# Kernel optimization log

Hardware: AMD Instinct MI355X
Metric: run time of the kernel (lower is better)

Reference implementation:

```python
import jax, jax.numpy as jnp
import numpy as np

EMBEDDING_DIM = 64
NUM_EMBEDDINGS = 512
COMMITMENT_COST = 0.25


def setup_inputs() -> dict:
    key = jax.random.key(0)
    k_x, k_w = jax.random.split(key)
    x = jax.random.normal(k_x, (32, 64, 64, EMBEDDING_DIM), dtype=jnp.float32)
    # he_normal initializer: stddev = sqrt(2 / fan_in), fan_in = embedding_dim
    emb_w = jax.random.normal(k_w, (NUM_EMBEDDINGS, EMBEDDING_DIM), dtype=jnp.float32) * jnp.sqrt(2.0 / EMBEDDING_DIM)
    return {"x": x, "emb_w": emb_w}


def reference(x, emb_w):
    D = emb_w.shape[1]
    K = emb_w.shape[0]
    flat = x.reshape(-1, D)  # [N, D]
    distances = (
        jnp.sum(flat * flat, axis=1, keepdims=True)
        - 2.0 * (flat @ emb_w.T)
        + jnp.sum(emb_w * emb_w, axis=1)[None, :]
    )
    # original: argmax(-distances) == argmin(distances)
    encoding_indices = jnp.argmin(distances, axis=1)  # [N]
    encodings = jax.nn.one_hot(encoding_indices, K, dtype=x.dtype)  # [N, K]
    quantized = emb_w[encoding_indices].reshape(x.shape)  # [B, H, W, D]

    sg = jax.lax.stop_gradient
    inp_latent_loss = jnp.mean((sg(quantized) - x) ** 2)
    emb_latent_loss = jnp.mean((quantized - sg(x)) ** 2)
    loss = emb_latent_loss + COMMITMENT_COST * inp_latent_loss

    # straight-through estimator
    quantized_st = x + sg(quantized - x)

    avg_probs = jnp.mean(encodings, axis=0)  # [K]
    perplexity = jnp.exp(-jnp.sum(avg_probs * jnp.log(avg_probs + 1e-10)))
    return (loss, quantized_st, perplexity, encodings)
```

## Files before the change

### kernel.cpp

```cpp
#include <hip/hip_runtime.h>
#include <math.h>

#define NVEC 131072
#define DIM 64
#define KCB 512
#define FLT_BIG 3.402823466e38f

typedef __attribute__((ext_vector_type(8))) short bf16x8;
typedef __attribute__((ext_vector_type(4))) float f32x4;
typedef __attribute__((ext_vector_type(2))) float f32x2;


__device__ inline unsigned int bf16_rne(float f) {
    unsigned int u = __float_as_uint(f);
    u += 0x7fffu + ((u >> 16) & 1u);
    return u >> 16;
}

__device__ inline void merge_top2(float& d1, int& i1, float& d2, int& i2) {
#pragma unroll
    for (int m = 16; m <= 32; m <<= 1) {
        float e1 = __shfl_xor(d1, m), e2 = __shfl_xor(d2, m);
        int j1 = __shfl_xor(i1, m), j2 = __shfl_xor(i2, m);
        bool af = (d1 < e1) || (d1 == e1 && i1 < j1);
        float w2 = af ? d2 : e2; int w2i = af ? i2 : j2;
        float lb = af ? e1 : d1; int lbi = af ? j1 : i1;
        bool bs = (w2 < lb) || (w2 == lb && w2i < lbi);
        d1 = af ? d1 : e1; i1 = af ? i1 : j1;
        d2 = bs ? w2 : lb; i2 = bs ? w2i : lbi;
    }
}

__global__ __launch_bounds__(256) void vq_prep(const float* __restrict__ emb,
                                               float* __restrict__ norms,
                                               unsigned short* __restrict__ e_bf2,
                                               unsigned int* __restrict__ counts,
                                               float* __restrict__ loss_acc) {
    int gid = blockIdx.x * 256 + threadIdx.x;
    int tt = gid >> 6, l = gid & 63;
    int nl = l & 15, kg = l >> 4;
    int row = tt * 16 + nl;
    const float* e = emb + row * DIM + kg * 8;

    float4 p0 = ((const float4*)e)[0];
    float4 p1 = ((const float4*)e)[1];
    float4 q0 = ((const float4*)(e + 32))[0];
    float4 q1 = ((const float4*)(e + 32))[1];

    float f0[8] = {p0.x, p0.y, p0.z, p0.w, p1.x, p1.y, p1.z, p1.w};
    float f1[8] = {q0.x, q0.y, q0.z, q0.w, q1.x, q1.y, q1.z, q1.w};

    float s = 0.f;
#pragma unroll
    for (int j = 0; j < 8; ++j) s = fmaf(f0[j], f0[j], fmaf(f1[j], f1[j], s));
    s += __shfl_xor(s, 16);
    s += __shfl_xor(s, 32);
    if (kg == 0) norms[row] = s;

    union { bf16x8 v; unsigned int u[4]; } H0, H1, L0, L1;
#pragma unroll
    for (int j = 0; j < 4; ++j) {
        unsigned int h0a = bf16_rne(f0[2 * j]),     h0b = bf16_rne(f0[2 * j + 1]);
        unsigned int h1a = bf16_rne(f1[2 * j]),     h1b = bf16_rne(f1[2 * j + 1]);
        float r0a = f0[2 * j] - __uint_as_float(h0a << 16);
        float r0b = f0[2 * j + 1] - __uint_as_float(h0b << 16);
        float r1a = f1[2 * j] - __uint_as_float(h1a << 16);
        float r1b = f1[2 * j + 1] - __uint_as_float(h1b << 16);
        H0.u[j] = h0a | (h0b << 16);
        H1.u[j] = h1a | (h1b << 16);
        L0.u[j] = bf16_rne(r0a) | (bf16_rne(r0b) << 16);
        L1.u[j] = bf16_rne(r1a) | (bf16_rne(r1b) << 16);
    }
    unsigned short* dst = e_bf2 + (size_t)tt * 8192 + l * 8;
    *(bf16x8*)(dst)        = H0.v;
    *(bf16x8*)(dst + 1024) = H1.v;
    *(bf16x8*)(dst + 2048) = L0.v;
    *(bf16x8*)(dst + 3072) = L1.v;

    if (gid < KCB) counts[gid] = 0u;
    if (gid == 0) *loss_acc = 0.f;
}

__global__ __launch_bounds__(256) void vq_fused(const float* __restrict__ x,
                                                const float* __restrict__ emb,
                                                const unsigned short* __restrict__ e_bf2,
                                                const float* __restrict__ norms,
                                                float* __restrict__ out,
                                                unsigned int* __restrict__ counts,
                                                float* __restrict__ loss_acc) {
    float* __restrict__ qout = out + 1;
    float* __restrict__ enc  = out + 8388610;
    int tid = threadIdx.x;
    int wave = tid >> 6;
    int lane = tid & 63;
    int nl = lane & 15, kg = lane >> 4;
    int rowA = blockIdx.x * 128 + wave * 32 + nl;
    int rowB = rowA + 16;

    __shared__ unsigned int hist[KCB];
    __shared__ int2 scand[128];
    __shared__ int sbi[128];
    __shared__ float serr[128];
    for (int j = tid; j < KCB; j += 256) hist[j] = 0u;

    bf16x8 xhA[2], xlA[2], xhB[2], xlB[2];
    {
        const float* xA = x + (size_t)rowA * DIM;
        const float* xB = x + (size_t)rowB * DIM;
#pragma unroll
        for (int ks = 0; ks < 2; ++ks) {
            const float4* pA = (const float4*)(xA + ks * 32 + kg * 8);
            const float4* pB = (const float4*)(xB + ks * 32 + kg * 8);
            float4 a0 = pA[0], a1 = pA[1], b0 = pB[0], b1 = pB[1];
            float fa[8] = {a0.x, a0.y, a0.z, a0.w, a1.x, a1.y, a1.z, a1.w};
            float fb[8] = {b0.x, b0.y, b0.z, b0.w, b1.x, b1.y, b1.z, b1.w};
            union { bf16x8 v; unsigned int u[4]; } HA, LA, HB, LB;
#pragma unroll
            for (int j = 0; j < 4; ++j) {
                unsigned int ha = bf16_rne(fa[2 * j]), hb = bf16_rne(fa[2 * j + 1]);
                unsigned int hc = bf16_rne(fb[2 * j]), hd = bf16_rne(fb[2 * j + 1]);
                float ra = fa[2 * j] - __uint_as_float(ha << 16);
                float rb = fa[2 * j + 1] - __uint_as_float(hb << 16);
                float rc = fb[2 * j] - __uint_as_float(hc << 16);
                float rd = fb[2 * j + 1] - __uint_as_float(hd << 16);
                HA.u[j] = ha | (hb << 16);
                LA.u[j] = bf16_rne(ra) | (bf16_rne(rb) << 16);
                HB.u[j] = hc | (hd << 16);
                LB.u[j] = bf16_rne(rc) | (bf16_rne(rd) << 16);
            }
            xhA[ks] = HA.v; xlA[ks] = LA.v;
            xhB[ks] = HB.v; xlB[ks] = LB.v;
        }
    }

    float d1A = FLT_BIG, d2A = FLT_BIG, d1B = FLT_BIG, d2B = FLT_BIG;
    int i1A = 0, i2A = 0, i1B = 0, i2B = 0;

    f32x2* enc2 = (f32x2*)enc;
    f32x4* enc4 = (f32x4*)(enc + 2);
    size_t zb4 = (size_t)blockIdx.x * 16384;
    f32x4 z4 = {0.f, 0.f, 0.f, 0.f};
    f32x2 z2 = {0.f, 0.f};
    if (tid == 0)   enc2[(size_t)blockIdx.x * 32768] = z2;
    if (tid == 255) enc2[(size_t)blockIdx.x * 32768 + 32767] = z2;

    int t0 = blockIdx.x & 31;
    const unsigned short* ebl = e_bf2 + (size_t)lane * 8;
#pragma unroll 2
    for (int t = 0; t < 32; ++t) {
        int tt = (t + t0) & 31;
        const unsigned short* eb = ebl + (size_t)tt * 8192;
        bf16x8 eh0 = *(const bf16x8*)(eb);
        bf16x8 eh1 = *(const bf16x8*)(eb + 1024);
        bf16x8 el0 = *(const bf16x8*)(eb + 2048);
        bf16x8 el1 = *(const bf16x8*)(eb + 3072);

        size_t s0 = zb4 + t * 512 + tid;
        enc4[s0] = z4;
        if (!(tid == 255 && t == 31)) enc4[s0 + 256] = z4;

        f32x4 aA0 = {}, aA1 = {}, aB0 = {}, aB1 = {};
        aA0 = __builtin_amdgcn_mfma_f32_16x16x32_bf16(eh0, xhA[0], aA0, 0, 0, 0);
        aA1 = __builtin_amdgcn_mfma_f32_16x16x32_bf16(eh1, xhA[1], aA1, 0, 0, 0);
        aB0 = __builtin_amdgcn_mfma_f32_16x16x32_bf16(eh0, xhB[0], aB0, 0, 0, 0);
        aB1 = __builtin_amdgcn_mfma_f32_16x16x32_bf16(eh1, xhB[1], aB1, 0, 0, 0);
        aA0 = __builtin_amdgcn_mfma_f32_16x16x32_bf16(el0, xhA[0], aA0, 0, 0, 0);
        aA1 = __builtin_amdgcn_mfma_f32_16x16x32_bf16(el1, xhA[1], aA1, 0, 0, 0);
        aB0 = __builtin_amdgcn_mfma_f32_16x16x32_bf16(el0, xhB[0], aB0, 0, 0, 0);
        aB1 = __builtin_amdgcn_mfma_f32_16x16x32_bf16(el1, xhB[1], aB1, 0, 0, 0);
        aA0 = __builtin_amdgcn_mfma_f32_16x16x32_bf16(eh0, xlA[0], aA0, 0, 0, 0);
        aA1 = __builtin_amdgcn_mfma_f32_16x16x32_bf16(eh1, xlA[1], aA1, 0, 0, 0);
        aB0 = __builtin_amdgcn_mfma_f32_16x16x32_bf16(eh0, xlB[0], aB0, 0, 0, 0);
        aB1 = __builtin_amdgcn_mfma_f32_16x16x32_bf16(eh1, xlB[1], aB1, 0, 0, 0);

        int krow0 = tt * 16 + kg * 4;
        f32x4 nv = *(const f32x4*)(norms + krow0);
#pragma unroll
        for (int r = 0; r < 4; ++r) {
            float en = nv[r];
            int ki = krow0 + r;
            float dA = fmaf(-2.f, aA0[r] + aA1[r], en);
            bool c1 = dA < d1A, c2 = dA < d2A;
            d2A = c1 ? d1A : (c2 ? dA : d2A);
            i2A = c1 ? i1A : (c2 ? ki : i2A);
            d1A = c1 ? dA : d1A;
            i1A = c1 ? ki : i1A;
            float dB = fmaf(-2.f, aB0[r] + aB1[r], en);
            bool e1c = dB < d1B, e2c = dB < d2B;
            d2B = e1c ? d1B : (e2c ? dB : d2B);
            i2B = e1c ? i1B : (e2c ? ki : i2B);
            d1B = e1c ? dB : d1B;
            i1B = e1c ? ki : i1B;
        }
    }

    merge_top2(d1A, i1A, d2A, i2A);
    merge_top2(d1B, i1B, d2B, i2B);
    if (lane < 16) {
        scand[wave * 32 + nl] = make_int2(i1A, i2A);
        scand[wave * 32 + nl + 16] = make_int2(i1B, i2B);
    }
    __syncthreads();

    if (tid < 128) {
        int grow = blockIdx.x * 128 + tid;
        int2 cd = scand[tid];
        const float4* xr = (const float4*)(x + (size_t)grow * DIM);
        const float4* eA = (const float4*)(emb + (size_t)cd.x * DIM);
        const float4* eB = (const float4*)(emb + (size_t)cd.y * DIM);

        float n0 = 0.f, n1 = 0.f, n2 = 0.f, n3 = 0.f;
        float a0 = 0.f, a1 = 0.f, a2 = 0.f, a3 = 0.f;
        float b0 = 0.f, b1 = 0.f, b2 = 0.f, b3 = 0.f;
#pragma unroll
        for (int j = 0; j < 16; ++j) {
            float4 xv = xr[j];
            float4 ev = eA[j], fv = eB[j];
            n0 = fmaf(xv.x, xv.x, n0);
            n1 = fmaf(xv.y, xv.y, n1);
            n2 = fmaf(xv.z, xv.z, n2);
            n3 = fmaf(xv.w, xv.w, n3);
            a0 = fmaf(xv.x, ev.x, a0);
            a1 = fmaf(xv.y, ev.y, a1);
            a2 = fmaf(xv.z, ev.z, a2);
            a3 = fmaf(xv.w, ev.w, a3);
            b0 = fmaf(xv.x, fv.x, b0);
            b1 = fmaf(xv.y, fv.y, b1);
            b2 = fmaf(xv.z, fv.z, b2);
            b3 = fmaf(xv.w, fv.w, b3);
        }
        float xn = (n0 + n1) + (n2 + n3);
        float dotA = (a0 + a1) + (a2 + a3);
        float dotB = (b0 + b1) + (b2 + b3);
        float dA = fmaf(-2.f, dotA, xn) + norms[cd.x];
        float dB = fmaf(-2.f, dotB, xn) + norms[cd.y];
        int bi = (dB < dA || (dB == dA && cd.y < cd.x)) ? cd.y : cd.x;

        const float4* ebv = (const float4*)(emb + (size_t)bi * DIM);
        float c0 = 0.f, c1 = 0.f, c2 = 0.f, c3 = 0.f;
#pragma unroll
        for (int j = 0; j < 16; ++j) {
            float4 xv = xr[j];
            float4 ev = ebv[j];
            float e0 = xv.x - ev.x, e1 = xv.y - ev.y;
            float e2 = xv.z - ev.z, e3 = xv.w - ev.w;
            c0 = fmaf(e0, e0, c0);
            c1 = fmaf(e1, e1, c1);
            c2 = fmaf(e2, e2, c2);
            c3 = fmaf(e3, e3, c3);
        }
        float err = (c0 + c1) + (c2 + c3);

        sbi[tid] = bi;
        serr[tid] = err;
        atomicAdd(&hist[bi], 1u);
        enc[(size_t)grow * KCB + bi] = 1.0f;
    }
    __syncthreads();

    for (int j = tid; j < KCB; j += 256) {
        unsigned int c = hist[j];
        if (c) atomicAdd(&counts[j], c);
    }
    if (tid < 64) {
        float v = serr[tid] + serr[tid + 64];
#pragma unroll
        for (int off = 32; off > 0; off >>= 1) v += __shfl_down(v, off);
        if (tid == 0) atomicAdd(loss_acc, v);
    }
#pragma unroll 4
    for (int j = 0; j < 32; ++j) {
        int f = j * 256 + tid;
        int r = f >> 6, c = f & 63;
        qout[((size_t)blockIdx.x * 128 + r) * DIM + c] =
            emb[(size_t)sbi[r] * DIM + c];
    }
}

__global__ __launch_bounds__(512) void vq_final(const unsigned int* __restrict__ counts,
                                                const float* __restrict__ loss_acc,
                                                float* __restrict__ out) {
    __shared__ float red[512];
    int t = threadIdx.x;
    float p = (float)counts[t] * (1.0f / 131072.0f);
    red[t] = p * logf(p + 1e-10f);
    __syncthreads();
    for (int s = 256; s > 0; s >>= 1) {
        if (t < s) red[t] += red[t + s];
        __syncthreads();
    }
    if (t == 0) {
        out[8388609] = expf(-red[0]);
        out[0] = 1.25f * (*loss_acc) * (1.0f / 8388608.0f);
    }
}

extern "C" void kernel_launch(void* const* d_in, const int* in_sizes, int n_in,
                              void* d_out, int out_size, void* d_ws, size_t ws_size,
                              hipStream_t stream) {
    const float* x   = (const float*)d_in[0];
    const float* emb = (const float*)d_in[1];
    float* out = (float*)d_out;
    char* ws = (char*)d_ws;
    unsigned int* counts = (unsigned int*)ws;
    float* loss_acc = (float*)(ws + 2048);
    float* norms = (float*)(ws + 4096);
    unsigned short* e_bf2 = (unsigned short*)(ws + 8192);

    vq_prep<<<8, 256, 0, stream>>>(emb, norms, e_bf2, counts, loss_acc);
    vq_fused<<<1024, 256, 0, stream>>>(x, emb, e_bf2, norms, out, counts, loss_acc);
    vq_final<<<1, 512, 0, stream>>>(counts, loss_acc, out);
}
```

Before: 90.46 us.

## Split one-hot zeroing into dedicated blocks and scatter ones in final kernel

The fused kernel previously zeroed its slice of the 256MB one-hot encoding output interleaved with the MFMA distance loop. Now odd blocks only stream zeros over the whole encoding buffer while even blocks do the quantization, and the winning indices go to a workspace array. A new final kernel scatters the 1.0 entries and also computes perplexity and loss. The aim is to decouple the bandwidth-bound zero fill from compute so both run at full rate. This costs an extra index round-trip and relies on kernel ordering so the ones are written after the zeros.

```diff
diff --git a/kernel.cpp b/kernel.cpp
--- a/kernel.cpp
+++ b/kernel.cpp
@@ -86,15 +86,30 @@
                                                 const unsigned short* __restrict__ e_bf2,
                                                 const float* __restrict__ norms,
                                                 float* __restrict__ out,
+                                                int* __restrict__ bi_out,
                                                 unsigned int* __restrict__ counts,
                                                 float* __restrict__ loss_acc) {
     float* __restrict__ qout = out + 1;
     float* __restrict__ enc  = out + 8388610;
+    int b = blockIdx.x;
     int tid = threadIdx.x;
+
+    if (b & 1) {
+        f32x4* enc4 = (f32x4*)(enc + 2);
+        int f = (b >> 1) * 256 + tid;
+        f32x4 z4 = {0.f, 0.f, 0.f, 0.f};
+#pragma unroll 4
+        for (int j = f; j < 16777215; j += 262144) enc4[j] = z4;
+        if (b == 1 && tid == 0) { enc[0] = 0.f; enc[1] = 0.f; }
+        if (b == 1 && tid == 1) { enc[67108862] = 0.f; enc[67108863] = 0.f; }
+        return;
+    }
+
+    int cb = b >> 1;
     int wave = tid >> 6;
     int lane = tid & 63;
     int nl = lane & 15, kg = lane >> 4;
-    int rowA = blockIdx.x * 128 + wave * 32 + nl;
+    int rowA = cb * 128 + wave * 32 + nl;
     int rowB = rowA + 16;
 
     __shared__ unsigned int hist[KCB];
@@ -136,15 +151,7 @@
     float d1A = FLT_BIG, d2A = FLT_BIG, d1B = FLT_BIG, d2B = FLT_BIG;
     int i1A = 0, i2A = 0, i1B = 0, i2B = 0;
 
-    f32x2* enc2 = (f32x2*)enc;
-    f32x4* enc4 = (f32x4*)(enc + 2);
-    size_t zb4 = (size_t)blockIdx.x * 16384;
-    f32x4 z4 = {0.f, 0.f, 0.f, 0.f};
-    f32x2 z2 = {0.f, 0.f};
-    if (tid == 0)   enc2[(size_t)blockIdx.x * 32768] = z2;
-    if (tid == 255) enc2[(size_t)blockIdx.x * 32768 + 32767] = z2;
-
-    int t0 = blockIdx.x & 31;
+    int t0 = cb & 31;
     const unsigned short* ebl = e_bf2 + (size_t)lane * 8;
 #pragma unroll 2
     for (int t = 0; t < 32; ++t) {
@@ -154,10 +161,6 @@
         bf16x8 eh1 = *(const bf16x8*)(eb + 1024);
         bf16x8 el0 = *(const bf16x8*)(eb + 2048);
         bf16x8 el1 = *(const bf16x8*)(eb + 3072);
-
-        size_t s0 = zb4 + t * 512 + tid;
-        enc4[s0] = z4;
-        if (!(tid == 255 && t == 31)) enc4[s0 + 256] = z4;
 
         f32x4 aA0 = {}, aA1 = {}, aB0 = {}, aB1 = {};
         aA0 = __builtin_amdgcn_mfma_f32_16x16x32_bf16(eh0, xhA[0], aA0, 0, 0, 0);
@@ -203,7 +206,7 @@
     __syncthreads();
 
     if (tid < 128) {
-        int grow = blockIdx.x * 128 + tid;
+        int grow = cb * 128 + tid;
         int2 cd = scand[tid];
         const float4* xr = (const float4*)(x + (size_t)grow * DIM);
         const float4* eA = (const float4*)(emb + (size_t)cd.x * DIM);
@@ -254,7 +257,7 @@
         sbi[tid] = bi;
         serr[tid] = err;
         atomicAdd(&hist[bi], 1u);
-        enc[(size_t)grow * KCB + bi] = 1.0f;
+        bi_out[grow] = bi;
     }
     __syncthreads();
 
@@ -272,26 +275,33 @@
     for (int j = 0; j < 32; ++j) {
         int f = j * 256 + tid;
         int r = f >> 6, c = f & 63;
-        qout[((size_t)blockIdx.x * 128 + r) * DIM + c] =
-            emb[(size_t)sbi[r] * DIM + c];
-    }
-}
-
-__global__ __launch_bounds__(512) void vq_final(const unsigned int* __restrict__ counts,
-                                                const float* __restrict__ loss_acc,
-                                                float* __restrict__ out) {
-    __shared__ float red[512];
-    int t = threadIdx.x;
-    float p = (float)counts[t] * (1.0f / 131072.0f);
-    red[t] = p * logf(p + 1e-10f);
-    __syncthreads();
-    for (int s = 256; s > 0; s >>= 1) {
-        if (t < s) red[t] += red[t + s];
+        qout[((size_t)cb * 128 + r) * DIM + c] = emb[(size_t)sbi[r] * DIM + c];
+    }
+}
+
+__global__ __launch_bounds__(256) void vq_sfin(const int* __restrict__ bi_idx,
+                                               const unsigned int* __restrict__ counts,
+                                               const float* __restrict__ loss_acc,
+                                               float* __restrict__ out) {
+    float* __restrict__ enc = out + 8388610;
+    int i = blockIdx.x * 256 + threadIdx.x;
+    enc[(size_t)i * KCB + bi_idx[i]] = 1.0f;
+
+    if (blockIdx.x == 0) {
+        __shared__ float red[256];
+        int t = threadIdx.x;
+        float pa = (float)counts[t] * (1.0f / 131072.0f);
+        float pb = (float)counts[t + 256] * (1.0f / 131072.0f);
+        red[t] = pa * logf(pa + 1e-10f) + pb * logf(pb + 1e-10f);
         __syncthreads();
-    }
-    if (t == 0) {
-        out[8388609] = expf(-red[0]);
-        out[0] = 1.25f * (*loss_acc) * (1.0f / 8388608.0f);
+        for (int s = 128; s > 0; s >>= 1) {
+            if (t < s) red[t] += red[t + s];
+            __syncthreads();
+        }
+        if (t == 0) {
+            out[8388609] = expf(-red[0]);
+            out[0] = 1.25f * (*loss_acc) * (1.0f / 8388608.0f);
+        }
     }
 }
 
@@ -306,8 +316,9 @@
     float* loss_acc = (float*)(ws + 2048);
     float* norms = (float*)(ws + 4096);
     unsigned short* e_bf2 = (unsigned short*)(ws + 8192);
+    int* bi_idx = (int*)(ws + 532480);
 
     vq_prep<<<8, 256, 0, stream>>>(emb, norms, e_bf2, counts, loss_acc);
-    vq_fused<<<1024, 256, 0, stream>>>(x, emb, e_bf2, norms, out, counts, loss_acc);
-    vq_final<<<1, 512, 0, stream>>>(counts, loss_acc, out);
-}
+    vq_fused<<<2048, 256, 0, stream>>>(x, emb, e_bf2, norms, out, bi_idx, counts, loss_acc);
+    vq_sfin<<<512, 256, 0, stream>>>(bi_idx, counts, loss_acc, out);
+}
```

Result: slower. 146.2 us (+61.6%).
